# Kernel tuning notes

Hardware: AMD Instinct MI355X
Metric: run time of the kernel (lower is better)

Reference implementation:

```python
import jax, jax.numpy as jnp
import numpy as np

TOP_K = 2
EPS = 1e-6


def setup_inputs() -> dict:
    key = jax.random.key(0)
    ks = jax.random.split(key, 8)
    B, S, D, E = 4, 2048, 2048, 8
    sd = 1.0 / np.sqrt(D)
    return {
        "x": jax.random.normal(ks[0], (B, S, D), dtype=jnp.float32),
        "Wr": jax.random.normal(ks[1], (D, E), dtype=jnp.float32) * sd,
        "br": jnp.zeros((E,), dtype=jnp.float32),
        "We": jax.random.normal(ks[2], (E, D, D), dtype=jnp.float32) * sd,
        "be": jnp.zeros((E, D), dtype=jnp.float32),
        "Wo": jax.random.normal(ks[3], (D, D), dtype=jnp.float32) * sd,
        "bo": jnp.zeros((D,), dtype=jnp.float32),
        "norm_w": jnp.ones((D,), dtype=jnp.float32),
    }


def reference(x, Wr, br, We, be, Wo, bo, norm_w):
    B, S, D = x.shape
    xf = x.reshape(-1, D)  # [T, D]
    # Router + top-k gating (softmax over the k selected logits, as in source)
    logits = xf @ Wr + br                      # [T, E]
    vals, idx = jax.lax.top_k(logits, TOP_K)   # [T, K]
    gates = jax.nn.softmax(vals, axis=-1)      # [T, K]
    # Expert FFN: Linear -> SiLU (dropout=0 -> identity). Dense over all experts,
    # then gather the top-k outputs per token.
    all_out = jax.nn.silu(jnp.einsum('td,edf->tef', xf, We) + be)  # [T, E, D]
    picked = jnp.take_along_axis(all_out, idx[:, :, None], axis=1)  # [T, K, D]
    combined = jnp.sum(gates[:, :, None] * picked, axis=1)          # [T, D]
    out = combined @ Wo + bo
    y = xf + out
    rms = jnp.sqrt(jnp.mean(y * y, axis=-1, keepdims=True) + EPS)
    return (norm_w * (y / rms)).reshape(B, S, D)
```

## Files before the change

### kernel.cpp

```cpp
#include <hip/hip_runtime.h>
#include <hip/hip_bf16.h>
#include <stdint.h>

typedef __bf16 bf16;
typedef __bf16 bf16x4 __attribute__((ext_vector_type(4)));
typedef __bf16 bf16x8 __attribute__((ext_vector_type(8)));
typedef float floatx4 __attribute__((ext_vector_type(4)));

#define T_TOK 8192
#define DIM 2048
#define NE 8
#define EPAD 2560
#define MAX_CHUNKS 136

__device__ inline void gld_lds16(const bf16* g, bf16* l) {
  __builtin_amdgcn_global_load_lds(
      (const __attribute__((address_space(1))) uint32_t*)g,
      (__attribute__((address_space(3))) uint32_t*)l, 16, 0, 0);
}

__global__ __launch_bounds__(256) void transpose_convert(
    const float* __restrict__ We, const float* __restrict__ Wo,
    bf16* __restrict__ We_t, bf16* __restrict__ Wo_t, int* __restrict__ cnt) {
  const int z = blockIdx.z;
  if (z == 8 && blockIdx.x == 0 && blockIdx.y == 0 && threadIdx.x < NE)
    cnt[threadIdx.x] = 0;
  const float* src = (z < 8) ? We + (size_t)z * DIM * DIM : Wo;
  bf16* dst = (z < 8) ? We_t + (size_t)z * DIM * DIM : Wo_t;
  __shared__ float tile[32][33];
  const int tx = threadIdx.x & 31;
  const int ty = threadIdx.x >> 5;
  const int n0 = blockIdx.x * 32;
  const int k0 = blockIdx.y * 32;
#pragma unroll
  for (int i = 0; i < 32; i += 8)
    tile[ty + i][tx] = src[(size_t)(k0 + ty + i) * DIM + n0 + tx];
  __syncthreads();
#pragma unroll
  for (int i = 0; i < 32; i += 8)
    dst[(size_t)(n0 + ty + i) * DIM + k0 + tx] = (bf16)tile[tx][ty + i];
}

__global__ __launch_bounds__(256) void router_kernel(
    const float* __restrict__ x, const float* __restrict__ Wr,
    const float* __restrict__ br, int* __restrict__ cnt,
    float* __restrict__ gate_list, int2* __restrict__ inv,
    bf16* __restrict__ xg) {
  const int t = blockIdx.x;
  const int tid = threadIdx.x;
  const float* xr = x + (size_t)t * DIM;
  float4 xv[2];
  float acc[8];
#pragma unroll
  for (int e = 0; e < 8; ++e) acc[e] = 0.f;
#pragma unroll
  for (int h = 0; h < 2; ++h) {
    const int d0 = tid * 4 + h * 1024;
    xv[h] = *(const float4*)&xr[d0];
    const float* wp = &Wr[(size_t)d0 * NE];
    float xe[4] = {xv[h].x, xv[h].y, xv[h].z, xv[h].w};
#pragma unroll
    for (int q = 0; q < 4; ++q) {
      float4 w0 = *(const float4*)&wp[q * 8];
      float4 w1 = *(const float4*)&wp[q * 8 + 4];
      acc[0] += xe[q] * w0.x; acc[1] += xe[q] * w0.y;
      acc[2] += xe[q] * w0.z; acc[3] += xe[q] * w0.w;
      acc[4] += xe[q] * w1.x; acc[5] += xe[q] * w1.y;
      acc[6] += xe[q] * w1.z; acc[7] += xe[q] * w1.w;
    }
  }
#pragma unroll
  for (int e = 0; e < 8; ++e) {
#pragma unroll
    for (int off = 32; off > 0; off >>= 1) acc[e] += __shfl_down(acc[e], off, 64);
  }
  __shared__ float red[4][8];
  __shared__ int sRow[2];
  const int lane = tid & 63, wid = tid >> 6;
  if (lane == 0) {
#pragma unroll
    for (int e = 0; e < 8; ++e) red[wid][e] = acc[e];
  }
  __syncthreads();
  if (tid == 0) {
    float lg[8];
#pragma unroll
    for (int e = 0; e < 8; ++e)
      lg[e] = red[0][e] + red[1][e] + red[2][e] + red[3][e] + br[e];
    int i0 = 0;
#pragma unroll
    for (int e = 1; e < 8; ++e) if (lg[e] > lg[i0]) i0 = e;
    int i1 = (i0 == 0) ? 1 : 0;
#pragma unroll
    for (int e = 0; e < 8; ++e)
      if (e != i0 && lg[e] > lg[i1]) i1 = e;
    const float g0 = 1.f / (1.f + expf(lg[i1] - lg[i0]));
    const float g1 = 1.f - g0;
    const int p0 = atomicAdd(&cnt[i0], 1);
    const int p1 = atomicAdd(&cnt[i1], 1);
    gate_list[i0 * T_TOK + p0] = g0;
    gate_list[i1 * T_TOK + p1] = g1;
    sRow[0] = i0 * EPAD + p0;
    sRow[1] = i1 * EPAD + p1;
    inv[t] = make_int2(sRow[0], sRow[1]);
  }
  __syncthreads();
  const size_t r0 = (size_t)sRow[0] * DIM;
  const size_t r1 = (size_t)sRow[1] * DIM;
#pragma unroll
  for (int h = 0; h < 2; ++h) {
    const int d0 = tid * 4 + h * 1024;
    bf16x4 xc;
    xc[0] = (bf16)xv[h].x; xc[1] = (bf16)xv[h].y;
    xc[2] = (bf16)xv[h].z; xc[3] = (bf16)xv[h].w;
    *(bf16x4*)&xg[r0 + d0] = xc;
    *(bf16x4*)&xg[r1 + d0] = xc;
  }
}


__global__ __launch_bounds__(256, 3) void expert_gemm(
    const bf16* __restrict__ xg, const bf16* __restrict__ Wt,
    const float* __restrict__ be, const int* __restrict__ cnt,
    const float* __restrict__ gate_list, bf16* __restrict__ aoutc) {
  const int cid = blockIdx.x;
  int e = -1, m0 = 0;
  {
    int acc = 0;
#pragma unroll
    for (int q = 0; q < NE; ++q) {
      const int c = (cnt[q] + 127) >> 7;
      if (e < 0 && cid < acc + c) { e = q; m0 = (cid - acc) * 128; }
      acc += c;
    }
  }
  if (e < 0) return;
  const int ne = cnt[e];
  const int n0 = blockIdx.y * 128;
  const int tid = threadIdx.x;

  __shared__ bf16 As[128 * 64];
  __shared__ bf16 Bs[128 * 64];
  __shared__ float gateS[128];

  if (tid < 128)
    gateS[tid] = (m0 + tid < ne) ? gate_list[e * T_TOK + m0 + tid] : 0.f;

  const int r0 = tid >> 3;
  const int kq = ((tid & 7) ^ (r0 & 7)) * 8;
  const bf16* wbase = Wt + (size_t)e * DIM * DIM;
  const bf16* abase = xg + (size_t)(e * EPAD + m0) * DIM;
  const bf16* ap[4];
  const bf16* bp[4];
#pragma unroll
  for (int h = 0; h < 4; ++h) {
    const int r = r0 + 32 * h;
    ap[h] = abase + (size_t)r * DIM + kq;
    bp[h] = wbase + (size_t)(n0 + r) * DIM + kq;
  }
  bf16* const asF = As;
  bf16* const bsF = Bs;

  const int lane = tid & 63, w = tid >> 6;
  const int wr = (w >> 1) * 64, wc = (w & 1) * 64;
  const int quad = lane >> 4, l15 = lane & 15;

  floatx4 acc[4][4];
#pragma unroll
  for (int i = 0; i < 4; ++i)
#pragma unroll
    for (int j = 0; j < 4; ++j) acc[i][j] = (floatx4){0.f, 0.f, 0.f, 0.f};

  int aoff[2][4], boff[2][4];
#pragma unroll
  for (int s = 0; s < 2; ++s) {
    const int kb = s * 4 + quad;
#pragma unroll
    for (int i = 0; i < 4; ++i) {
      const int mi = wr + i * 16 + l15;
      aoff[s][i] = mi * 64 + ((kb ^ (mi & 7)) * 8);
      const int nj = wc + i * 16 + l15;
      boff[s][i] = nj * 64 + ((kb ^ (nj & 7)) * 8);
    }
  }

  for (int k0 = 0; k0 < DIM; k0 += 64) {
#pragma unroll
    for (int h = 0; h < 4; ++h) {
      gld_lds16(bp[h] + k0, bsF + ((size_t)tid + 256 * h) * 8);
      gld_lds16(ap[h] + k0, asF + ((size_t)tid + 256 * h) * 8);
    }
    __syncthreads();
#pragma unroll
    for (int s = 0; s < 2; ++s) {
      bf16x8 af[4], bfr[4];
#pragma unroll
      for (int i = 0; i < 4; ++i) af[i] = *(const bf16x8*)&asF[aoff[s][i]];
#pragma unroll
      for (int j = 0; j < 4; ++j) bfr[j] = *(const bf16x8*)&bsF[boff[s][j]];
#pragma unroll
      for (int i = 0; i < 4; ++i)
#pragma unroll
        for (int j = 0; j < 4; ++j)
          acc[i][j] = __builtin_amdgcn_mfma_f32_16x16x32_bf16(af[i], bfr[j], acc[i][j], 0, 0, 0);
    }
    __syncthreads();
  }

#pragma unroll
  for (int j = 0; j < 4; ++j) {
    const int col = n0 + wc + j * 16 + l15;
    const float bev = be[e * DIM + col];
#pragma unroll
    for (int i = 0; i < 4; ++i) {
#pragma unroll
      for (int r = 0; r < 4; ++r) {
        const int rl = wr + i * 16 + quad * 4 + r;
        if (m0 + rl < ne) {
          float v = acc[i][j][r] + bev;
          v = v / (1.f + __expf(-v));
          v *= gateS[rl];
          aoutc[(size_t)(e * EPAD + m0 + rl) * DIM + col] = (bf16)v;
        }
      }
    }
  }
}

__global__ __launch_bounds__(256, 3) void proj_gemm(
    const bf16* __restrict__ aoutc, const bf16* __restrict__ Wot,
    const int2* __restrict__ inv, const float* __restrict__ bo,
    const float* __restrict__ x, float* __restrict__ y) {
  const int m0 = blockIdx.x * 128;
  const int n0 = blockIdx.y * 128;
  const int tid = threadIdx.x;

  __shared__ bf16 As[128 * 64];
  __shared__ bf16 Bs[128 * 64];

  const int r0 = tid >> 3;
  const int kq = ((tid & 7) ^ (r0 & 7)) * 8;
  const bf16* a0[4];
  const bf16* a1[4];
  const bf16* bp[4];
#pragma unroll
  for (int h = 0; h < 4; ++h) {
    const int r = r0 + 32 * h;
    const int2 iv = inv[m0 + r];
    a0[h] = aoutc + (size_t)iv.x * DIM + kq;
    a1[h] = aoutc + (size_t)iv.y * DIM + kq;
    bp[h] = Wot + (size_t)(n0 + r) * DIM + kq;
  }
  bf16* const asF = As;
  bf16* const bsF = Bs;

  const int lane = tid & 63, w = tid >> 6;
  const int wr = (w >> 1) * 64, wc = (w & 1) * 64;
  const int quad = lane >> 4, l15 = lane & 15;

  floatx4 acc[4][4];
#pragma unroll
  for (int i = 0; i < 4; ++i)
#pragma unroll
    for (int j = 0; j < 4; ++j) acc[i][j] = (floatx4){0.f, 0.f, 0.f, 0.f};

  int aoff[2][4], boff[2][4];
#pragma unroll
  for (int s = 0; s < 2; ++s) {
    const int kb = s * 4 + quad;
#pragma unroll
    for (int i = 0; i < 4; ++i) {
      const int mi = wr + i * 16 + l15;
      aoff[s][i] = mi * 64 + ((kb ^ (mi & 7)) * 8);
      const int nj = wc + i * 16 + l15;
      boff[s][i] = nj * 64 + ((kb ^ (nj & 7)) * 8);
    }
  }

  for (int k0 = 0; k0 < DIM; k0 += 64) {
#pragma unroll
    for (int h = 0; h < 4; ++h)
      gld_lds16(bp[h] + k0, bsF + ((size_t)tid + 256 * h) * 8);
    bf16x8 u0[4], u1[4];
#pragma unroll
    for (int h = 0; h < 4; ++h) {
      u0[h] = *(const bf16x8*)(a0[h] + k0);
      u1[h] = *(const bf16x8*)(a1[h] + k0);
    }
#pragma unroll
    for (int h = 0; h < 4; ++h) {
      bf16x8 s;
#pragma unroll
      for (int q = 0; q < 8; ++q)
        s[q] = (bf16)((float)u0[h][q] + (float)u1[h][q]);
      *(bf16x8*)&asF[((size_t)tid + 256 * h) * 8] = s;
    }
    __syncthreads();
#pragma unroll
    for (int s = 0; s < 2; ++s) {
      bf16x8 af[4], bfr[4];
#pragma unroll
      for (int i = 0; i < 4; ++i) af[i] = *(const bf16x8*)&asF[aoff[s][i]];
#pragma unroll
      for (int j = 0; j < 4; ++j) bfr[j] = *(const bf16x8*)&bsF[boff[s][j]];
#pragma unroll
      for (int i = 0; i < 4; ++i)
#pragma unroll
        for (int j = 0; j < 4; ++j)
          acc[i][j] = __builtin_amdgcn_mfma_f32_16x16x32_bf16(af[i], bfr[j], acc[i][j], 0, 0, 0);
    }
    __syncthreads();
  }

#pragma unroll
  for (int j = 0; j < 4; ++j) {
    const int col = n0 + wc + j * 16 + l15;
    const float bov = bo[col];
#pragma unroll
    for (int i = 0; i < 4; ++i) {
#pragma unroll
      for (int r = 0; r < 4; ++r) {
        const int rl = wr + i * 16 + quad * 4 + r;
        const size_t o = (size_t)(m0 + rl) * DIM + col;
        y[o] = acc[i][j][r] + bov + x[o];
      }
    }
  }
}

__global__ __launch_bounds__(256) void rmsnorm_kernel(
    float* __restrict__ y, const float* __restrict__ w) {
  const int row = blockIdx.x;
  const int tid = threadIdx.x;
  float* yr = y + (size_t)row * DIM;
  float4 v0 = ((const float4*)yr)[tid];
  float4 v1 = ((const float4*)yr)[tid + 256];
  float ss = v0.x * v0.x + v0.y * v0.y + v0.z * v0.z + v0.w * v0.w +
             v1.x * v1.x + v1.y * v1.y + v1.z * v1.z + v1.w * v1.w;
#pragma unroll
  for (int off = 32; off > 0; off >>= 1) ss += __shfl_down(ss, off, 64);
  __shared__ float s4[4];
  const int lane = tid & 63, wid = tid >> 6;
  if (lane == 0) s4[wid] = ss;
  __syncthreads();
  const float tot = s4[0] + s4[1] + s4[2] + s4[3];
  const float r = rsqrtf(tot / (float)DIM + 1e-6f);
  float4 w0 = ((const float4*)w)[tid];
  float4 w1 = ((const float4*)w)[tid + 256];
  float4 o0 = make_float4(v0.x * r * w0.x, v0.y * r * w0.y, v0.z * r * w0.z, v0.w * r * w0.w);
  float4 o1 = make_float4(v1.x * r * w1.x, v1.y * r * w1.y, v1.z * r * w1.z, v1.w * r * w1.w);
  ((float4*)yr)[tid] = o0;
  ((float4*)yr)[tid + 256] = o1;
}

extern "C" void kernel_launch(void* const* d_in, const int* in_sizes, int n_in,
                              void* d_out, int out_size, void* d_ws, size_t ws_size,
                              hipStream_t stream) {
  const float* x  = (const float*)d_in[0];
  const float* Wr = (const float*)d_in[1];
  const float* br = (const float*)d_in[2];
  const float* We = (const float*)d_in[3];
  const float* be = (const float*)d_in[4];
  const float* Wo = (const float*)d_in[5];
  const float* bo = (const float*)d_in[6];
  const float* nw = (const float*)d_in[7];
  float* out = (float*)d_out;

  uint8_t* ws = (uint8_t*)d_ws;
  size_t off = 0;
  auto carve = [&](size_t bytes) -> void* {
    void* p = ws + off;
    off += (bytes + 255) & ~(size_t)255;
    return p;
  };
  int*   cnt       = (int*)carve(NE * sizeof(int));
  float* gate_list = (float*)carve((size_t)NE * T_TOK * sizeof(float));
  int2*  inv       = (int2*)carve((size_t)T_TOK * sizeof(int2));
  bf16*  We_t      = (bf16*)carve((size_t)NE * DIM * DIM * sizeof(bf16));
  bf16*  Wo_t      = (bf16*)carve((size_t)DIM * DIM * sizeof(bf16));
  bf16*  xg        = (bf16*)carve((size_t)NE * EPAD * DIM * sizeof(bf16));
  bf16*  aoutc     = (bf16*)carve((size_t)NE * EPAD * DIM * sizeof(bf16));
  (void)ws_size; (void)in_sizes; (void)n_in; (void)out_size;

  transpose_convert<<<dim3(DIM / 32, DIM / 32, NE + 1), 256, 0, stream>>>(
      We, Wo, We_t, Wo_t, cnt);
  router_kernel<<<T_TOK, 256, 0, stream>>>(x, Wr, br, cnt, gate_list, inv, xg);
  expert_gemm<<<dim3(MAX_CHUNKS, DIM / 128), 256, 0, stream>>>(
      xg, We_t, be, cnt, gate_list, aoutc);
  proj_gemm<<<dim3(T_TOK / 128, DIM / 128), 256, 0, stream>>>(
      aoutc, Wo_t, inv, bo, x, out);
  rmsnorm_kernel<<<T_TOK, 256, 0, stream>>>(out, nw);
}
```

Before: 853.8 us.

## Rework GEMMs to 256x256 double-buffered pipelined tiles and split combine kernel

```diff
diff --git a/kernel.cpp b/kernel.cpp
--- a/kernel.cpp
+++ b/kernel.cpp
@@ -11,7 +11,8 @@
 #define DIM 2048
 #define NE 8
 #define EPAD 2560
-#define MAX_CHUNKS 136
+#define NTIL (DIM / 64)
+#define MAXC 72
 
 __device__ inline void gld_lds16(const bf16* g, bf16* l) {
   __builtin_amdgcn_global_load_lds(
@@ -27,18 +28,23 @@
     cnt[threadIdx.x] = 0;
   const float* src = (z < 8) ? We + (size_t)z * DIM * DIM : Wo;
   bf16* dst = (z < 8) ? We_t + (size_t)z * DIM * DIM : Wo_t;
-  __shared__ float tile[32][33];
-  const int tx = threadIdx.x & 31;
-  const int ty = threadIdx.x >> 5;
-  const int n0 = blockIdx.x * 32;
-  const int k0 = blockIdx.y * 32;
-#pragma unroll
-  for (int i = 0; i < 32; i += 8)
-    tile[ty + i][tx] = src[(size_t)(k0 + ty + i) * DIM + n0 + tx];
+  __shared__ float tile[64][65];
+  const int tx = threadIdx.x & 63, ty = threadIdx.x >> 6;
+  const int n0 = blockIdx.x * 64, k0 = blockIdx.y * 64;
+#pragma unroll
+  for (int i = 0; i < 16; ++i)
+    tile[ty + 4 * i][tx] = src[(size_t)(k0 + ty + 4 * i) * DIM + n0 + tx];
   __syncthreads();
-#pragma unroll
-  for (int i = 0; i < 32; i += 8)
-    dst[(size_t)(n0 + ty + i) * DIM + k0 + tx] = (bf16)tile[tx][ty + i];
+  const int kc = (threadIdx.x & 15) * 4;
+  const int nrb = threadIdx.x >> 4;
+#pragma unroll
+  for (int p = 0; p < 4; ++p) {
+    const int nr = nrb + 16 * p;
+    bf16x4 v;
+#pragma unroll
+    for (int q = 0; q < 4; ++q) v[q] = (bf16)tile[kc + q][nr];
+    *(bf16x4*)&dst[(size_t)(n0 + nr) * DIM + k0 + kc] = v;
+  }
 }
 
 __global__ __launch_bounds__(256) void router_kernel(
@@ -119,31 +125,142 @@
 }
 
 
-__global__ __launch_bounds__(256, 3) void expert_gemm(
+#define TILE_BODY(LAST)                                                       \
+  {                                                                           \
+    const bf16* asF = &As[p][0];                                              \
+    const bf16* bsF = &Bs[p][0];                                              \
+    bf16* asN = &As[p ^ 1][0];                                                \
+    bf16* bsN = &Bs[p ^ 1][0];                                                \
+    const int kn = (t + 1) * 64;                                              \
+    bf16x8 af[4][2], b01[2][2], b23[2][2];                                    \
+                    \
+    asm volatile("s_waitcnt vmcnt(2)" ::: "memory");                          \
+    __builtin_amdgcn_s_barrier();                                             \
+    _Pragma("unroll") for (int i = 0; i < 4; ++i) {                           \
+      af[i][0] = *(const bf16x8*)&asF[aoff[i] + xs0];                         \
+      af[i][1] = *(const bf16x8*)&asF[aoff[i] + xs1];                         \
+    }                                                                         \
+    _Pragma("unroll") for (int j = 0; j < 2; ++j) {                           \
+      b01[j][0] = *(const bf16x8*)&bsF[boff[j] + xs0];                        \
+      b01[j][1] = *(const bf16x8*)&bsF[boff[j] + xs1];                        \
+    }                                                                         \
+    if (!(LAST)) {                                                            \
+      gld_lds16(ap[0] + kn, asN + (size_t)tid * 8);                           \
+      gld_lds16(ap[2] + kn, asN + (size_t)(1024 + tid) * 8);                  \
+    }                                                                         \
+    __builtin_amdgcn_s_setprio(1);                                            \
+    _Pragma("unroll") for (int s = 0; s < 2; ++s)                             \
+      _Pragma("unroll") for (int i = 0; i < 4; ++i)                           \
+        _Pragma("unroll") for (int j = 0; j < 2; ++j)                         \
+          acc[i][j] = __builtin_amdgcn_mfma_f32_16x16x32_bf16(                \
+              af[i][s], b01[j][s], acc[i][j], 0, 0, 0);                       \
+    __builtin_amdgcn_s_setprio(0);                                            \
+                    \
+    __builtin_amdgcn_s_barrier();                                             \
+    _Pragma("unroll") for (int j = 0; j < 2; ++j) {                           \
+      b23[j][0] = *(const bf16x8*)&bsF[boff[j + 2] + xs0];                    \
+      b23[j][1] = *(const bf16x8*)&bsF[boff[j + 2] + xs1];                    \
+    }                                                                         \
+    if (!(LAST)) {                                                            \
+      gld_lds16(bp[0] + kn, bsN + (size_t)tid * 8);                           \
+      gld_lds16(bp[1] + kn, bsN + (size_t)(512 + tid) * 8);                   \
+    }                                                                         \
+    __builtin_amdgcn_s_setprio(1);                                            \
+    _Pragma("unroll") for (int s = 0; s < 2; ++s)                             \
+      _Pragma("unroll") for (int i = 0; i < 4; ++i)                           \
+        _Pragma("unroll") for (int j = 0; j < 2; ++j)                         \
+          acc[i][j + 2] = __builtin_amdgcn_mfma_f32_16x16x32_bf16(            \
+              af[i][s], b23[j][s], acc[i][j + 2], 0, 0, 0);                   \
+    __builtin_amdgcn_s_setprio(0);                                            \
+                   \
+    if (LAST) { asm volatile("s_waitcnt vmcnt(0)" ::: "memory"); }            \
+    else      { asm volatile("s_waitcnt vmcnt(4)" ::: "memory"); }            \
+    __builtin_amdgcn_s_barrier();                                             \
+    _Pragma("unroll") for (int i = 0; i < 4; ++i) {                           \
+      af[i][0] = *(const bf16x8*)&asF[aoff[i + 4] + xs0];                     \
+      af[i][1] = *(const bf16x8*)&asF[aoff[i + 4] + xs1];                     \
+    }                                                                         \
+    if (!(LAST)) {                                                            \
+      gld_lds16(bp[2] + kn, bsN + (size_t)(1024 + tid) * 8);                  \
+      gld_lds16(bp[3] + kn, bsN + (size_t)(1536 + tid) * 8);                  \
+    }                                                                         \
+    __builtin_amdgcn_s_setprio(1);                                            \
+    _Pragma("unroll") for (int s = 0; s < 2; ++s)                             \
+      _Pragma("unroll") for (int i = 0; i < 4; ++i)                           \
+        _Pragma("unroll") for (int j = 0; j < 2; ++j)                         \
+          acc[i + 4][j + 2] = __builtin_amdgcn_mfma_f32_16x16x32_bf16(        \
+              af[i][s], b23[j][s], acc[i + 4][j + 2], 0, 0, 0);               \
+    __builtin_amdgcn_s_setprio(0);                                            \
+                   \
+    __builtin_amdgcn_s_barrier();                                             \
+    if (!(LAST)) {                                                            \
+      gld_lds16(ap[1] + kn, asN + (size_t)(512 + tid) * 8);                   \
+      gld_lds16(ap[3] + kn, asN + (size_t)(1536 + tid) * 8);                  \
+    }                                                                         \
+    __builtin_amdgcn_s_setprio(1);                                            \
+    _Pragma("unroll") for (int s = 0; s < 2; ++s)                             \
+      _Pragma("unroll") for (int i = 0; i < 4; ++i)                           \
+        _Pragma("unroll") for (int j = 0; j < 2; ++j)                         \
+          acc[i + 4][j] = __builtin_amdgcn_mfma_f32_16x16x32_bf16(            \
+              af[i][s], b01[j][s], acc[i + 4][j], 0, 0, 0);                   \
+    __builtin_amdgcn_s_setprio(0);                                            \
+    p ^= 1;                                                                   \
+  }
+
+#define GEMM_SETUP_FRAGS()                                                    \
+  const int lane = tid & 63, w = tid >> 6;                                    \
+  const int wm = w >> 2, wn = w & 3;                                          \
+  const int quad = lane >> 4, l15 = lane & 15;                                \
+  const int xs0 = ((quad) ^ (l15 & 7)) * 8;                                   \
+  const int xs1 = ((quad + 4) ^ (l15 & 7)) * 8;                               \
+  int aoff[8], boff[4];                                                       \
+  _Pragma("unroll") for (int i = 0; i < 8; ++i)                               \
+      aoff[i] = (wm * 128 + i * 16 + l15) * 64;                               \
+  _Pragma("unroll") for (int j = 0; j < 4; ++j)                               \
+      boff[j] = (wn * 64 + j * 16 + l15) * 64;                                \
+  floatx4 acc[8][4];                                                          \
+  _Pragma("unroll") for (int i = 0; i < 8; ++i)                               \
+    _Pragma("unroll") for (int j = 0; j < 4; ++j)                             \
+        acc[i][j] = (floatx4){0.f, 0.f, 0.f, 0.f};
+
+#define GEMM_PROLOGUE()                                                       \
+  gld_lds16(ap[0], &As[0][(size_t)tid * 8]);                                  \
+  gld_lds16(ap[2], &As[0][(size_t)(1024 + tid) * 8]);                         \
+  gld_lds16(bp[0], &Bs[0][(size_t)tid * 8]);                                  \
+  gld_lds16(bp[1], &Bs[0][(size_t)(512 + tid) * 8]);                          \
+  gld_lds16(bp[2], &Bs[0][(size_t)(1024 + tid) * 8]);                         \
+  gld_lds16(bp[3], &Bs[0][(size_t)(1536 + tid) * 8]);                         \
+  gld_lds16(ap[1], &As[0][(size_t)(512 + tid) * 8]);                          \
+  gld_lds16(ap[3], &As[0][(size_t)(1536 + tid) * 8]);                         \
+  int p = 0;                                                                  \
+  int t = 0;                                                                  \
+  for (; t < NTIL - 1; ++t) TILE_BODY(0);                                     \
+  TILE_BODY(1);
+
+__global__ __launch_bounds__(512, 2) void expert_gemm(
     const bf16* __restrict__ xg, const bf16* __restrict__ Wt,
     const float* __restrict__ be, const int* __restrict__ cnt,
     const float* __restrict__ gate_list, bf16* __restrict__ aoutc) {
-  const int cid = blockIdx.x;
-  int e = -1, m0 = 0;
-  {
-    int acc = 0;
-#pragma unroll
-    for (int q = 0; q < NE; ++q) {
-      const int c = (cnt[q] + 127) >> 7;
-      if (e < 0 && cid < acc + c) { e = q; m0 = (cid - acc) * 128; }
-      acc += c;
-    }
-  }
-  if (e < 0) return;
+  const int b = blockIdx.x;
+  const int wg = (b & 7) * MAXC + (b >> 3);
+  const int cid = wg >> 3;
+  int e = -1, m0 = 0, total = 0;
+#pragma unroll
+  for (int q = 0; q < NE; ++q) {
+    const int c = (cnt[q] + 255) >> 8;
+    if (e < 0 && cid < total + c) { e = q; m0 = (cid - total) * 256; }
+    total += c;
+  }
+  if (e < 0 || cid >= total) return;
   const int ne = cnt[e];
-  const int n0 = blockIdx.y * 128;
+  const int n0 = (wg & 7) * 256;
   const int tid = threadIdx.x;
 
-  __shared__ bf16 As[128 * 64];
-  __shared__ bf16 Bs[128 * 64];
-  __shared__ float gateS[128];
-
-  if (tid < 128)
+  __shared__ bf16 As[2][256 * 64];
+  __shared__ bf16 Bs[2][256 * 64];
+  __shared__ float gateS[256];
+
+  if (tid < 256)
     gateS[tid] = (m0 + tid < ne) ? gate_list[e * T_TOK + m0 + tid] : 0.f;
 
   const int r0 = tid >> 3;
@@ -154,68 +271,23 @@
   const bf16* bp[4];
 #pragma unroll
   for (int h = 0; h < 4; ++h) {
-    const int r = r0 + 32 * h;
+    const int r = r0 + 64 * h;
     ap[h] = abase + (size_t)r * DIM + kq;
     bp[h] = wbase + (size_t)(n0 + r) * DIM + kq;
   }
-  bf16* const asF = As;
-  bf16* const bsF = Bs;
-
-  const int lane = tid & 63, w = tid >> 6;
-  const int wr = (w >> 1) * 64, wc = (w & 1) * 64;
-  const int quad = lane >> 4, l15 = lane & 15;
-
-  floatx4 acc[4][4];
-#pragma unroll
-  for (int i = 0; i < 4; ++i)
-#pragma unroll
-    for (int j = 0; j < 4; ++j) acc[i][j] = (floatx4){0.f, 0.f, 0.f, 0.f};
-
-  int aoff[2][4], boff[2][4];
-#pragma unroll
-  for (int s = 0; s < 2; ++s) {
-    const int kb = s * 4 + quad;
-#pragma unroll
-    for (int i = 0; i < 4; ++i) {
-      const int mi = wr + i * 16 + l15;
-      aoff[s][i] = mi * 64 + ((kb ^ (mi & 7)) * 8);
-      const int nj = wc + i * 16 + l15;
-      boff[s][i] = nj * 64 + ((kb ^ (nj & 7)) * 8);
-    }
-  }
-
-  for (int k0 = 0; k0 < DIM; k0 += 64) {
-#pragma unroll
-    for (int h = 0; h < 4; ++h) {
-      gld_lds16(bp[h] + k0, bsF + ((size_t)tid + 256 * h) * 8);
-      gld_lds16(ap[h] + k0, asF + ((size_t)tid + 256 * h) * 8);
-    }
-    __syncthreads();
-#pragma unroll
-    for (int s = 0; s < 2; ++s) {
-      bf16x8 af[4], bfr[4];
-#pragma unroll
-      for (int i = 0; i < 4; ++i) af[i] = *(const bf16x8*)&asF[aoff[s][i]];
-#pragma unroll
-      for (int j = 0; j < 4; ++j) bfr[j] = *(const bf16x8*)&bsF[boff[s][j]];
-#pragma unroll
-      for (int i = 0; i < 4; ++i)
-#pragma unroll
-        for (int j = 0; j < 4; ++j)
-          acc[i][j] = __builtin_amdgcn_mfma_f32_16x16x32_bf16(af[i], bfr[j], acc[i][j], 0, 0, 0);
-    }
-    __syncthreads();
-  }
+
+  GEMM_SETUP_FRAGS()
+  GEMM_PROLOGUE()
 
 #pragma unroll
   for (int j = 0; j < 4; ++j) {
-    const int col = n0 + wc + j * 16 + l15;
+    const int col = n0 + wn * 64 + j * 16 + l15;
     const float bev = be[e * DIM + col];
 #pragma unroll
-    for (int i = 0; i < 4; ++i) {
+    for (int i = 0; i < 8; ++i) {
 #pragma unroll
       for (int r = 0; r < 4; ++r) {
-        const int rl = wr + i * 16 + quad * 4 + r;
+        const int rl = wm * 128 + i * 16 + quad * 4 + r;
         if (m0 + rl < ne) {
           float v = acc[i][j][r] + bev;
           v = v / (1.f + __expf(-v));
@@ -227,100 +299,56 @@
   }
 }
 
-__global__ __launch_bounds__(256, 3) void proj_gemm(
-    const bf16* __restrict__ aoutc, const bf16* __restrict__ Wot,
-    const int2* __restrict__ inv, const float* __restrict__ bo,
-    const float* __restrict__ x, float* __restrict__ y) {
-  const int m0 = blockIdx.x * 128;
-  const int n0 = blockIdx.y * 128;
+__global__ __launch_bounds__(256) void combine_kernel(
+    const bf16* __restrict__ aoutc, const int2* __restrict__ inv,
+    bf16* __restrict__ hcomb) {
+  const int t = blockIdx.x;
+  const int2 iv = inv[t];
+  const int d = threadIdx.x * 8;
+  bf16x8 u0 = *(const bf16x8*)&aoutc[(size_t)iv.x * DIM + d];
+  bf16x8 u1 = *(const bf16x8*)&aoutc[(size_t)iv.y * DIM + d];
+  bf16x8 s;
+#pragma unroll
+  for (int q = 0; q < 8; ++q) s[q] = (bf16)((float)u0[q] + (float)u1[q]);
+  *(bf16x8*)&hcomb[(size_t)t * DIM + d] = s;
+}
+
+__global__ __launch_bounds__(512, 2) void proj_gemm(
+    const bf16* __restrict__ hcomb, const bf16* __restrict__ Wot,
+    const float* __restrict__ bo, const float* __restrict__ x,
+    float* __restrict__ y) {
+  const int b = blockIdx.x;
+  const int wg = (b & 7) * 32 + (b >> 3);
+  const int m0 = (wg >> 3) * 256;
+  const int n0 = (wg & 7) * 256;
   const int tid = threadIdx.x;
 
-  __shared__ bf16 As[128 * 64];
-  __shared__ bf16 Bs[128 * 64];
+  __shared__ bf16 As[2][256 * 64];
+  __shared__ bf16 Bs[2][256 * 64];
 
   const int r0 = tid >> 3;
   const int kq = ((tid & 7) ^ (r0 & 7)) * 8;
-  const bf16* a0[4];
-  const bf16* a1[4];
+  const bf16* ap[4];
   const bf16* bp[4];
 #pragma unroll
   for (int h = 0; h < 4; ++h) {
-    const int r = r0 + 32 * h;
-    const int2 iv = inv[m0 + r];
-    a0[h] = aoutc + (size_t)iv.x * DIM + kq;
-    a1[h] = aoutc + (size_t)iv.y * DIM + kq;
+    const int r = r0 + 64 * h;
+    ap[h] = hcomb + (size_t)(m0 + r) * DIM + kq;
     bp[h] = Wot + (size_t)(n0 + r) * DIM + kq;
   }
-  bf16* const asF = As;
-  bf16* const bsF = Bs;
-
-  const int lane = tid & 63, w = tid >> 6;
-  const int wr = (w >> 1) * 64, wc = (w & 1) * 64;
-  const int quad = lane >> 4, l15 = lane & 15;
-
-  floatx4 acc[4][4];
-#pragma unroll
-  for (int i = 0; i < 4; ++i)
-#pragma unroll
-    for (int j = 0; j < 4; ++j) acc[i][j] = (floatx4){0.f, 0.f, 0.f, 0.f};
-
-  int aoff[2][4], boff[2][4];
-#pragma unroll
-  for (int s = 0; s < 2; ++s) {
-    const int kb = s * 4 + quad;
-#pragma unroll
-    for (int i = 0; i < 4; ++i) {
-      const int mi = wr + i * 16 + l15;
-      aoff[s][i] = mi * 64 + ((kb ^ (mi & 7)) * 8);
-      const int nj = wc + i * 16 + l15;
-      boff[s][i] = nj * 64 + ((kb ^ (nj & 7)) * 8);
-    }
-  }
-
-  for (int k0 = 0; k0 < DIM; k0 += 64) {
-#pragma unroll
-    for (int h = 0; h < 4; ++h)
-      gld_lds16(bp[h] + k0, bsF + ((size_t)tid + 256 * h) * 8);
-    bf16x8 u0[4], u1[4];
-#pragma unroll
-    for (int h = 0; h < 4; ++h) {
-      u0[h] = *(const bf16x8*)(a0[h] + k0);
-      u1[h] = *(const bf16x8*)(a1[h] + k0);
-    }
-#pragma unroll
-    for (int h = 0; h < 4; ++h) {
-      bf16x8 s;
-#pragma unroll
-      for (int q = 0; q < 8; ++q)
-        s[q] = (bf16)((float)u0[h][q] + (float)u1[h][q]);
-      *(bf16x8*)&asF[((size_t)tid + 256 * h) * 8] = s;
-    }
-    __syncthreads();
-#pragma unroll
-    for (int s = 0; s < 2; ++s) {
-      bf16x8 af[4], bfr[4];
-#pragma unroll
-      for (int i = 0; i < 4; ++i) af[i] = *(const bf16x8*)&asF[aoff[s][i]];
-#pragma unroll
-      for (int j = 0; j < 4; ++j) bfr[j] = *(const bf16x8*)&bsF[boff[s][j]];
-#pragma unroll
-      for (int i = 0; i < 4; ++i)
-#pragma unroll
-        for (int j = 0; j < 4; ++j)
-          acc[i][j] = __builtin_amdgcn_mfma_f32_16x16x32_bf16(af[i], bfr[j], acc[i][j], 0, 0, 0);
-    }
-    __syncthreads();
-  }
+
+  GEMM_SETUP_FRAGS()
+  GEMM_PROLOGUE()
 
 #pragma unroll
   for (int j = 0; j < 4; ++j) {
-    const int col = n0 + wc + j * 16 + l15;
+    const int col = n0 + wn * 64 + j * 16 + l15;
     const float bov = bo[col];
 #pragma unroll
-    for (int i = 0; i < 4; ++i) {
+    for (int i = 0; i < 8; ++i) {
 #pragma unroll
       for (int r = 0; r < 4; ++r) {
-        const int rl = wr + i * 16 + quad * 4 + r;
+        const int rl = wm * 128 + i * 16 + quad * 4 + r;
         const size_t o = (size_t)(m0 + rl) * DIM + col;
         y[o] = acc[i][j][r] + bov + x[o];
       }
@@ -380,14 +408,13 @@
   bf16*  Wo_t      = (bf16*)carve((size_t)DIM * DIM * sizeof(bf16));
   bf16*  xg        = (bf16*)carve((size_t)NE * EPAD * DIM * sizeof(bf16));
   bf16*  aoutc     = (bf16*)carve((size_t)NE * EPAD * DIM * sizeof(bf16));
+  bf16*  hcomb     = We_t;
   (void)ws_size; (void)in_sizes; (void)n_in; (void)out_size;
 
-  transpose_convert<<<dim3(DIM / 32, DIM / 32, NE + 1), 256, 0, stream>>>(
-      We, Wo, We_t, Wo_t, cnt);
+  transpose_convert<<<dim3(32, 32, 9), 256, 0, stream>>>(We, Wo, We_t, Wo_t, cnt);
   router_kernel<<<T_TOK, 256, 0, stream>>>(x, Wr, br, cnt, gate_list, inv, xg);
-  expert_gemm<<<dim3(MAX_CHUNKS, DIM / 128), 256, 0, stream>>>(
-      xg, We_t, be, cnt, gate_list, aoutc);
-  proj_gemm<<<dim3(T_TOK / 128, DIM / 128), 256, 0, stream>>>(
-      aoutc, Wo_t, inv, bo, x, out);
+  expert_gemm<<<dim3(MAXC * 8), 512, 0, stream>>>(xg, We_t, be, cnt, gate_list, aoutc);
+  combine_kernel<<<T_TOK, 256, 0, stream>>>(aoutc, inv, hcomb);
+  proj_gemm<<<dim3(32 * 8), 512, 0, stream>>>(hcomb, Wo_t, bo, x, out);
   rmsnorm_kernel<<<T_TOK, 256, 0, stream>>>(out, nw);
 }
```

New measurement: 842.1 us. About the same (-1.4%).
